# Optimization experiments

Hardware: AMD Instinct MI355X
Metric: run time of the kernel (lower is better)

The kernel has to match this reference:

```python
import jax, jax.numpy as jnp
import numpy as np

S = 100   # n_pred_samples
B = 64    # batch
DIMS = [784, 512, 512, 10]


def setup_inputs() -> dict:
    key = jax.random.key(0)
    ks = jax.random.split(key, 16)
    d = {}
    d["inputs"] = jax.random.normal(ks[0], (B, DIMS[0]), dtype=jnp.float32)
    d["task_id"] = 0
    # variational params: means ~ 0.1*N(0,1), logvars constant -6 (as in module init)
    d["wm0"] = jax.random.normal(ks[1], (DIMS[0], DIMS[1])) * 0.1
    d["wv0"] = jnp.full((DIMS[0], DIMS[1]), -6.0, jnp.float32)
    d["bm0"] = jnp.full((DIMS[1],), 0.1, jnp.float32)
    d["bv0"] = jnp.full((DIMS[1],), -6.0, jnp.float32)
    d["wm1"] = jax.random.normal(ks[2], (DIMS[1], DIMS[2])) * 0.1
    d["wv1"] = jnp.full((DIMS[1], DIMS[2]), -6.0, jnp.float32)
    d["bm1"] = jnp.full((DIMS[2],), 0.1, jnp.float32)
    d["bv1"] = jnp.full((DIMS[2],), -6.0, jnp.float32)
    d["wml"] = jax.random.normal(ks[3], (DIMS[2], DIMS[3])) * 0.1
    d["wvl"] = jnp.full((DIMS[2], DIMS[3]), -6.0, jnp.float32)
    d["bml"] = jnp.full((DIMS[3],), 0.1, jnp.float32)
    d["bvl"] = jnp.full((DIMS[3],), -6.0, jnp.float32)
    # reparameterization noise (passed explicitly for determinism)
    d["we0"] = jax.random.normal(ks[4], (S, DIMS[0], DIMS[1]), dtype=jnp.float32)
    d["be0"] = jax.random.normal(ks[5], (S, 1, DIMS[1]), dtype=jnp.float32)
    d["we1"] = jax.random.normal(ks[6], (S, DIMS[1], DIMS[2]), dtype=jnp.float32)
    d["be1"] = jax.random.normal(ks[7], (S, 1, DIMS[2]), dtype=jnp.float32)
    d["wel"] = jax.random.normal(ks[8], (S, DIMS[2], DIMS[3]), dtype=jnp.float32)
    d["bel"] = jax.random.normal(ks[9], (S, 1, DIMS[3]), dtype=jnp.float32)
    return d


def _sample(eps, logvar, mean):
    # reparameterization: eps * exp(0.5*logvar) + mean
    return eps * jnp.exp(0.5 * logvar) + mean


def reference(inputs, task_id, wm0, wv0, bm0, bv0, wm1, wv1, bm1, bv1,
              wml, wvl, bml, bvl, we0, be0, we1, be1, wel, bel):
    # activations: [S, B, D]
    act = jnp.broadcast_to(inputs[None], (S,) + inputs.shape)
    # hidden layer 0
    W0 = _sample(we0, wv0, wm0)          # [S, D0, D1]
    b0 = _sample(be0, bv0, bm0)          # [S, 1, D1]
    act = jax.nn.relu(jnp.einsum('sbi,sio->sbo', act, W0) + b0)
    # hidden layer 1
    W1 = _sample(we1, wv1, wm1)
    b1 = _sample(be1, bv1, bm1)
    act = jax.nn.relu(jnp.einsum('sbi,sio->sbo', act, W1) + b1)
    # last (task-specific) layer: original does broadcast-mul + sum over dim 2,
    # which is exactly a batched matmul — expressed here as an einsum
    Wl = _sample(wel, wvl, wml)          # [S, D2, O]
    bl = _sample(bel, bvl, bml)          # [S, 1, O]
    logits = jnp.einsum('sbh,sho->sbo', act, Wl) + bl   # [S, B, O]
    return logits
```

## Files before the change

kernel.cpp:

```cpp
#include <hip/hip_runtime.h>
#include <hip/hip_bf16.h>


typedef __bf16 bf16x8 __attribute__((ext_vector_type(8)));
typedef float f32x4 __attribute__((ext_vector_type(4)));

#define NSAMP 100
#define BATCH 64
#define D0 784
#define D1 512
#define D2 512
#define DOUT 10
#define K0PAD 800

__device__ __forceinline__ unsigned short f2bf(float f) {
    __bf16 b = (__bf16)f;
    return __builtin_bit_cast(unsigned short, b);
}
__device__ __forceinline__ float bf_hi(unsigned int u) {
    return __builtin_bit_cast(float, u & 0xffff0000u);
}
__device__ __forceinline__ float bf_lo(unsigned int u) {
    return __builtin_bit_cast(float, u << 16);
}

union FragU { uint2 d[2]; uint4 q; bf16x8 v; };

#define XB_N   (BATCH * K0PAD)
#define PS0_N  (D0 * D1)
#define PS1_N  (D1 * D2)
#define SGL_N  (D2 * DOUT)
#define B0_N   (NSAMP * D1)
#define B1_N   (NSAMP * D2)
#define BL_N   (NSAMP * DOUT)
#define PREP_TOTAL (XB_N + PS0_N + PS1_N + SGL_N + B0_N + B1_N + BL_N)

__global__ __launch_bounds__(256) void prep(
    const float* __restrict__ inputs,
    const float* __restrict__ wv0, const float* __restrict__ wm0,
    const float* __restrict__ wv1, const float* __restrict__ wm1,
    const float* __restrict__ wvl,
    const float* __restrict__ be0, const float* __restrict__ bv0, const float* __restrict__ bm0,
    const float* __restrict__ be1, const float* __restrict__ bv1, const float* __restrict__ bm1,
    const float* __restrict__ bel, const float* __restrict__ bvl, const float* __restrict__ bml,
    unsigned short* __restrict__ Xb,
    unsigned int* __restrict__ psm0, unsigned int* __restrict__ psm1,
    float* __restrict__ sigmal,
    float* __restrict__ bias0, float* __restrict__ bias1, float* __restrict__ biasl)
{
    int i = blockIdx.x * 256 + threadIdx.x;
    if (i < XB_N) {
        int m = i / K0PAD, k = i % K0PAD;
        float v = (k < D0) ? inputs[m * D0 + k] : 0.f;
        Xb[i] = f2bf(v);
        return;
    }
    i -= XB_N;
    if (i < PS0_N) {
        unsigned int sg = f2bf(__expf(0.5f * wv0[i]));
        unsigned int mn = f2bf(wm0[i]);
        psm0[i] = (sg << 16) | mn;
        return;
    }
    i -= PS0_N;
    if (i < PS1_N) {
        unsigned int sg = f2bf(__expf(0.5f * wv1[i]));
        unsigned int mn = f2bf(wm1[i]);
        psm1[i] = (sg << 16) | mn;
        return;
    }
    i -= PS1_N;
    if (i < SGL_N) { sigmal[i] = __expf(0.5f * wvl[i]); return; }
    i -= SGL_N;
    if (i < B0_N) { int n = i % D1; bias0[i] = fmaf(be0[i], __expf(0.5f * bv0[n]), bm0[n]); return; }
    i -= B0_N;
    if (i < B1_N) { int n = i % D2; bias1[i] = fmaf(be1[i], __expf(0.5f * bv1[n]), bm1[n]); return; }
    i -= B1_N;
    if (i < BL_N) { int o = i % DOUT; biasl[i] = fmaf(bel[i], __expf(0.5f * bvl[o]), bml[o]); return; }
}

__global__ __launch_bounds__(256) void gemm_wave(
    const unsigned short* __restrict__ A, int lda, long aStride,
    const float* __restrict__ eps, long eStride,
    const unsigned int* __restrict__ psm,
    int KT, int Kvalid,
    const float* __restrict__ bias,
    void* __restrict__ outp, int outBf16)
{
    const int N = 512;
    const int wid  = blockIdx.x * 4 + (threadIdx.x >> 6);
    const int s    = wid >> 5;
    const int n0   = (wid & 31) << 4;
    const int lane = threadIdx.x & 63;
    const int fr   = lane & 15;
    const int quad = lane >> 4;

    const unsigned short* aP = A + (long)s * aStride + (long)fr * lda + quad * 8;
    const long bbase = (long)(quad * 8) * N + n0 + fr;
    const float* eP        = eps + (long)s * eStride + bbase;
    const unsigned int* pP = psm + bbase;

    f32x4 acc[4] = {};
    const bool tail = (Kvalid < KT * 32);

    uint4 pa0[4], pa1[4];
    float pe0[8], pe1[8];
    unsigned int pp0[8], pp1[8];

    auto loadAll = [&](int kt, uint4* pa, float* pe, unsigned int* pp) {
        const int kb = kt * 32;
        const bool guard = tail && (kt == KT - 1);
#pragma unroll
        for (int sub = 0; sub < 4; ++sub)
            pa[sub] = *reinterpret_cast<const uint4*>(aP + (long)sub * 16 * lda + kb);
#pragma unroll
        for (int j = 0; j < 8; ++j) {
            const long off = (long)(kb + j) * N;
            const bool ok = !guard || (kb + quad * 8 + j) < Kvalid;
            pe[j] = ok ? __builtin_nontemporal_load(eP + off) : 0.f;
            pp[j] = ok ? pP[off] : 0u;
        }
    };

    auto compute = [&](const uint4* pa, const float* pe, const unsigned int* pp) {
        unsigned int u[4];
#pragma unroll
        for (int h = 0; h < 4; ++h) {
            float w0 = fmaf(pe[2 * h],     bf_hi(pp[2 * h]),     bf_lo(pp[2 * h]));
            float w1 = fmaf(pe[2 * h + 1], bf_hi(pp[2 * h + 1]), bf_lo(pp[2 * h + 1]));
            u[h] = (unsigned int)f2bf(w0) | ((unsigned int)f2bf(w1) << 16);
        }
        FragU bf;
        bf.d[0].x = u[0]; bf.d[0].y = u[1];
        bf.d[1].x = u[2]; bf.d[1].y = u[3];
#pragma unroll
        for (int sub = 0; sub < 4; ++sub) {
            FragU af; af.q = pa[sub];
            acc[sub] = __builtin_amdgcn_mfma_f32_16x16x32_bf16(af.v, bf.v, acc[sub], 0, 0, 0);
        }
    };

    loadAll(0, pa0, pe0, pp0);
    int kt = 0;
    for (; kt + 2 <= KT; kt += 2) {
        loadAll(kt + 1, pa1, pe1, pp1);
        compute(pa0, pe0, pp0);
        if (kt + 2 < KT) loadAll(kt + 2, pa0, pe0, pp0);
        compute(pa1, pe1, pp1);
    }
    if (kt < KT) compute(pa0, pe0, pp0);

    const float bv = bias[(long)s * N + n0 + fr];
    const long outBase = (long)s * BATCH * N;
#pragma unroll
    for (int sub = 0; sub < 4; ++sub) {
#pragma unroll
        for (int r = 0; r < 4; ++r) {
            const int row = sub * 16 + quad * 4 + r;
            float v = acc[sub][r] + bv;
            v = fmaxf(v, 0.f);
            const long idx = outBase + (long)row * N + n0 + fr;
            if (outBf16) ((unsigned short*)outp)[idx] = f2bf(v);
            else         ((float*)outp)[idx] = v;
        }
    }
}

__global__ __launch_bounds__(320) void last_layer(
    const float* __restrict__ act2,
    const float* __restrict__ wel,
    const float* __restrict__ sigmal,
    const float* __restrict__ wml,
    const float* __restrict__ biasl,
    float* __restrict__ out)
{
    __shared__ float smW[D2 * DOUT];
    const int s = blockIdx.x;
    const int t = threadIdx.x;
    const float* we = wel + (long)s * D2 * DOUT;
    for (int i = t; i < D2 * DOUT; i += 320)
        smW[i] = fmaf(we[i], sigmal[i], wml[i]);
    __syncthreads();

    const int m  = t / 5;
    const int op = t % 5;
    const float* a = act2 + ((long)s * BATCH + m) * D2;
    float acc0 = 0.f, acc1 = 0.f;
#pragma unroll 4
    for (int k = 0; k < D2; k += 4) {
        float4 av = *reinterpret_cast<const float4*>(a + k);
        acc0 = fmaf(av.x, smW[(k + 0) * DOUT + op], acc0);
        acc0 = fmaf(av.y, smW[(k + 1) * DOUT + op], acc0);
        acc0 = fmaf(av.z, smW[(k + 2) * DOUT + op], acc0);
        acc0 = fmaf(av.w, smW[(k + 3) * DOUT + op], acc0);
        acc1 = fmaf(av.x, smW[(k + 0) * DOUT + op + 5], acc1);
        acc1 = fmaf(av.y, smW[(k + 1) * DOUT + op + 5], acc1);
        acc1 = fmaf(av.z, smW[(k + 2) * DOUT + op + 5], acc1);
        acc1 = fmaf(av.w, smW[(k + 3) * DOUT + op + 5], acc1);
    }
    const long ob = ((long)s * BATCH + m) * DOUT;
    out[ob + op]     = acc0 + biasl[s * DOUT + op];
    out[ob + op + 5] = acc1 + biasl[s * DOUT + op + 5];
}

extern "C" void kernel_launch(void* const* d_in, const int* in_sizes, int n_in,
                              void* d_out, int out_size, void* d_ws, size_t ws_size,
                              hipStream_t stream)
{
    const float* inputs = (const float*)d_in[0];
    const float* wm0 = (const float*)d_in[2];
    const float* wv0 = (const float*)d_in[3];
    const float* bm0 = (const float*)d_in[4];
    const float* bv0 = (const float*)d_in[5];
    const float* wm1 = (const float*)d_in[6];
    const float* wv1 = (const float*)d_in[7];
    const float* bm1 = (const float*)d_in[8];
    const float* bv1 = (const float*)d_in[9];
    const float* wml = (const float*)d_in[10];
    const float* wvl = (const float*)d_in[11];
    const float* bml = (const float*)d_in[12];
    const float* bvl = (const float*)d_in[13];
    const float* we0 = (const float*)d_in[14];
    const float* be0 = (const float*)d_in[15];
    const float* we1 = (const float*)d_in[16];
    const float* be1 = (const float*)d_in[17];
    const float* wel = (const float*)d_in[18];
    const float* bel = (const float*)d_in[19];

    char* w = (char*)d_ws;
    unsigned short* Xb  = (unsigned short*)w; w += (size_t)XB_N * 2;
    unsigned int* psm0  = (unsigned int*)w;   w += (size_t)PS0_N * 4;
    unsigned int* psm1  = (unsigned int*)w;   w += (size_t)PS1_N * 4;
    float* sigmal = (float*)w; w += (size_t)SGL_N * 4;
    float* bias0  = (float*)w; w += (size_t)B0_N * 4;
    float* bias1  = (float*)w; w += (size_t)B1_N * 4;
    float* biasl  = (float*)w; w += (size_t)BL_N * 4;
    unsigned short* act1 = (unsigned short*)w; w += (size_t)NSAMP * BATCH * D1 * 2;
    float* act2 = (float*)w; w += (size_t)NSAMP * BATCH * D2 * 4;

    prep<<<dim3((PREP_TOTAL + 255) / 256), 256, 0, stream>>>(
        inputs, wv0, wm0, wv1, wm1, wvl,
        be0, bv0, bm0, be1, bv1, bm1, bel, bvl, bml,
        Xb, psm0, psm1, sigmal, bias0, bias1, biasl);

    gemm_wave<<<dim3(NSAMP * 32 / 4), 256, 0, stream>>>(
        Xb, K0PAD, 0L, we0, (long)D0 * D1, psm0,
        K0PAD / 32, D0, bias0, (void*)act1, 1);

    gemm_wave<<<dim3(NSAMP * 32 / 4), 256, 0, stream>>>(
        act1, D1, (long)BATCH * D1, we1, (long)D1 * D2, psm1,
        D1 / 32, D1, bias1, (void*)act2, 0);

    last_layer<<<dim3(NSAMP), 320, 0, stream>>>(
        act2, wel, sigmal, wml, biasl, (float*)d_out);
}
```

Before: 456.9 us.

## Widen gemm wave tile to 32 columns with vectorized eps loads and LDS transpose

```diff
diff --git a/kernel.cpp b/kernel.cpp
--- a/kernel.cpp
+++ b/kernel.cpp
@@ -12,6 +12,7 @@
 #define D2 512
 #define DOUT 10
 #define K0PAD 800
+#define RSB 40
 
 __device__ __forceinline__ unsigned short f2bf(float f) {
     __bf16 b = (__bf16)f;
@@ -24,7 +25,7 @@
     return __builtin_bit_cast(float, u << 16);
 }
 
-union FragU { uint2 d[2]; uint4 q; bf16x8 v; };
+union FragU { uint4 q; bf16x8 v; };
 
 #define XB_N   (BATCH * K0PAD)
 #define PS0_N  (D0 * D1)
@@ -79,7 +80,7 @@
     if (i < BL_N) { int o = i % DOUT; biasl[i] = fmaf(bel[i], __expf(0.5f * bvl[o]), bml[o]); return; }
 }
 
-__global__ __launch_bounds__(256) void gemm_wave(
+__global__ __launch_bounds__(64) void gemm_wave(
     const unsigned short* __restrict__ A, int lda, long aStride,
     const float* __restrict__ eps, long eStride,
     const unsigned int* __restrict__ psm,
@@ -87,81 +88,101 @@
     const float* __restrict__ bias,
     void* __restrict__ outp, int outBf16)
 {
-    const int N = 512;
-    const int wid  = blockIdx.x * 4 + (threadIdx.x >> 6);
-    const int s    = wid >> 5;
-    const int n0   = (wid & 31) << 4;
-    const int lane = threadIdx.x & 63;
-    const int fr   = lane & 15;
-    const int quad = lane >> 4;
+    __shared__ unsigned short smB[32 * RSB];
+
+    const int bx = blockIdx.x;
+    const int s  = bx >> 4;
+    const int n0 = (bx & 15) << 5;
+    const int l  = threadIdx.x;
+    const int fr = l & 15, quad = l >> 4;
+    const int kg = l >> 3;
+    const int ng = l & 7;
 
     const unsigned short* aP = A + (long)s * aStride + (long)fr * lda + quad * 8;
-    const long bbase = (long)(quad * 8) * N + n0 + fr;
-    const float* eP        = eps + (long)s * eStride + bbase;
-    const unsigned int* pP = psm + bbase;
-
-    f32x4 acc[4] = {};
-    const bool tail = (Kvalid < KT * 32);
-
-    uint4 pa0[4], pa1[4];
-    float pe0[8], pe1[8];
-    unsigned int pp0[8], pp1[8];
-
-    auto loadAll = [&](int kt, uint4* pa, float* pe, unsigned int* pp) {
+    const float* eB        = eps + (long)s * eStride + n0 + 4 * ng;
+    const unsigned int* pB = psm + n0 + 4 * ng;
+
+    f32x4 acc[4][2] = {};
+
+    float4 ea0[4], ea1[4];
+    uint4  pa0[4], pa1[4], aa0[4], aa1[4];
+
+    auto loadAll = [&](int kt, float4* ea, uint4* pa, uint4* aa) {
         const int kb = kt * 32;
-        const bool guard = tail && (kt == KT - 1);
-#pragma unroll
-        for (int sub = 0; sub < 4; ++sub)
-            pa[sub] = *reinterpret_cast<const uint4*>(aP + (long)sub * 16 * lda + kb);
-#pragma unroll
-        for (int j = 0; j < 8; ++j) {
-            const long off = (long)(kb + j) * N;
-            const bool ok = !guard || (kb + quad * 8 + j) < Kvalid;
-            pe[j] = ok ? __builtin_nontemporal_load(eP + off) : 0.f;
-            pp[j] = ok ? pP[off] : 0u;
+#pragma unroll
+        for (int mi = 0; mi < 4; ++mi)
+            aa[mi] = *reinterpret_cast<const uint4*>(aP + (long)(mi * 16) * lda + kb);
+#pragma unroll
+        for (int j = 0; j < 4; ++j) {
+            const int row = kb + 4 * kg + j;
+            const bool ok = row < Kvalid;
+            const long off = (long)(ok ? row : 0) * 512;
+            float4 e = *reinterpret_cast<const float4*>(eB + off);
+            uint4  p = *reinterpret_cast<const uint4*>(pB + off);
+            if (!ok) { e = float4{0.f, 0.f, 0.f, 0.f}; p = uint4{0u, 0u, 0u, 0u}; }
+            ea[j] = e; pa[j] = p;
         }
     };
 
-    auto compute = [&](const uint4* pa, const float* pe, const unsigned int* pp) {
-        unsigned int u[4];
-#pragma unroll
-        for (int h = 0; h < 4; ++h) {
-            float w0 = fmaf(pe[2 * h],     bf_hi(pp[2 * h]),     bf_lo(pp[2 * h]));
-            float w1 = fmaf(pe[2 * h + 1], bf_hi(pp[2 * h + 1]), bf_lo(pp[2 * h + 1]));
-            u[h] = (unsigned int)f2bf(w0) | ((unsigned int)f2bf(w1) << 16);
-        }
-        FragU bf;
-        bf.d[0].x = u[0]; bf.d[0].y = u[1];
-        bf.d[1].x = u[2]; bf.d[1].y = u[3];
-#pragma unroll
-        for (int sub = 0; sub < 4; ++sub) {
-            FragU af; af.q = pa[sub];
-            acc[sub] = __builtin_amdgcn_mfma_f32_16x16x32_bf16(af.v, bf.v, acc[sub], 0, 0, 0);
+    auto stage = [&](const float4* ea, const uint4* pa) {
+        float w[4][4];
+#pragma unroll
+        for (int j = 0; j < 4; ++j) {
+            w[j][0] = fmaf(ea[j].x, bf_hi(pa[j].x), bf_lo(pa[j].x));
+            w[j][1] = fmaf(ea[j].y, bf_hi(pa[j].y), bf_lo(pa[j].y));
+            w[j][2] = fmaf(ea[j].z, bf_hi(pa[j].z), bf_lo(pa[j].z));
+            w[j][3] = fmaf(ea[j].w, bf_hi(pa[j].w), bf_lo(pa[j].w));
+        }
+#pragma unroll
+        for (int i = 0; i < 4; ++i) {
+            uint2 d;
+            d.x = (unsigned)f2bf(w[0][i]) | ((unsigned)f2bf(w[1][i]) << 16);
+            d.y = (unsigned)f2bf(w[2][i]) | ((unsigned)f2bf(w[3][i]) << 16);
+            *reinterpret_cast<uint2*>(&smB[(4 * ng + i) * RSB + 4 * kg]) = d;
         }
     };
 
-    loadAll(0, pa0, pe0, pp0);
+    auto compute = [&](const uint4* aa) {
+        FragU bf0, bf1;
+        bf0.q = *reinterpret_cast<const uint4*>(&smB[fr * RSB + quad * 8]);
+        bf1.q = *reinterpret_cast<const uint4*>(&smB[(16 + fr) * RSB + quad * 8]);
+#pragma unroll
+        for (int mi = 0; mi < 4; ++mi) {
+            FragU af; af.q = aa[mi];
+            acc[mi][0] = __builtin_amdgcn_mfma_f32_16x16x32_bf16(af.v, bf0.v, acc[mi][0], 0, 0, 0);
+            acc[mi][1] = __builtin_amdgcn_mfma_f32_16x16x32_bf16(af.v, bf1.v, acc[mi][1], 0, 0, 0);
+        }
+    };
+
+    loadAll(0, ea0, pa0, aa0);
     int kt = 0;
     for (; kt + 2 <= KT; kt += 2) {
-        loadAll(kt + 1, pa1, pe1, pp1);
-        compute(pa0, pe0, pp0);
-        if (kt + 2 < KT) loadAll(kt + 2, pa0, pe0, pp0);
-        compute(pa1, pe1, pp1);
-    }
-    if (kt < KT) compute(pa0, pe0, pp0);
-
-    const float bv = bias[(long)s * N + n0 + fr];
-    const long outBase = (long)s * BATCH * N;
-#pragma unroll
-    for (int sub = 0; sub < 4; ++sub) {
-#pragma unroll
-        for (int r = 0; r < 4; ++r) {
-            const int row = sub * 16 + quad * 4 + r;
-            float v = acc[sub][r] + bv;
-            v = fmaxf(v, 0.f);
-            const long idx = outBase + (long)row * N + n0 + fr;
-            if (outBf16) ((unsigned short*)outp)[idx] = f2bf(v);
-            else         ((float*)outp)[idx] = v;
+        loadAll(kt + 1, ea1, pa1, aa1);
+        stage(ea0, pa0);
+        compute(aa0);
+        if (kt + 2 < KT) loadAll(kt + 2, ea0, pa0, aa0);
+        stage(ea1, pa1);
+        compute(aa1);
+    }
+    if (kt < KT) { stage(ea0, pa0); compute(aa0); }
+
+    const float bv0v = bias[(long)s * 512 + n0 + fr];
+    const float bv1v = bias[(long)s * 512 + n0 + 16 + fr];
+    const long outBase = (long)s * BATCH * 512;
+#pragma unroll
+    for (int mi = 0; mi < 4; ++mi) {
+#pragma unroll
+        for (int ni = 0; ni < 2; ++ni) {
+            const float bv = ni ? bv1v : bv0v;
+            const int col = n0 + ni * 16 + fr;
+#pragma unroll
+            for (int r = 0; r < 4; ++r) {
+                const int row = mi * 16 + quad * 4 + r;
+                float v = fmaxf(acc[mi][ni][r] + bv, 0.f);
+                const long idx = outBase + (long)row * 512 + col;
+                if (outBf16) ((unsigned short*)outp)[idx] = f2bf(v);
+                else         ((float*)outp)[idx] = v;
+            }
         }
     }
 }
@@ -243,11 +264,11 @@
         be0, bv0, bm0, be1, bv1, bm1, bel, bvl, bml,
         Xb, psm0, psm1, sigmal, bias0, bias1, biasl);
 
-    gemm_wave<<<dim3(NSAMP * 32 / 4), 256, 0, stream>>>(
+    gemm_wave<<<dim3(NSAMP * 16), 64, 0, stream>>>(
         Xb, K0PAD, 0L, we0, (long)D0 * D1, psm0,
         K0PAD / 32, D0, bias0, (void*)act1, 1);
 
-    gemm_wave<<<dim3(NSAMP * 32 / 4), 256, 0, stream>>>(
+    gemm_wave<<<dim3(NSAMP * 16), 64, 0, stream>>>(
         act1, D1, (long)BATCH * D1, we1, (long)D1 * D2, psm1,
         D1 / 32, D1, bias1, (void*)act2, 0);
 
```

Result: faster. 406.9 us (-10.9%).
